# Kernel tuning notes

Hardware: AMD Instinct MI355X
Metric: run time of the kernel (lower is better)

The kernel has to match this reference:

```python
import jax, jax.numpy as jnp
import numpy as np

MAX_DISP = 48


def setup_inputs() -> dict:
    key = jax.random.key(0)
    k1, k2 = jax.random.split(key)
    n, c, h, w = 2, 32, 136, 240
    left = jax.random.normal(k1, (n, c, h, w), dtype=jnp.float32)
    right = jax.random.normal(k2, (n, c, h, w), dtype=jnp.float32)
    return {"left": left, "right": right}


def _cost_volume(left, right, max_disp):
    # volume[n, c, d, h, w] = left[n,c,h,w] * right[n,c,h,w-d] for w >= d, else 0
    w = left.shape[-1]
    slices = []
    for d in range(max_disp):
        # shift right feature map by d along W, zero-padding on the left;
        # the zero pad makes volume[..., :d] zero automatically, matching the
        # torch loop that only writes volume[:, :, d, :, d:].
        shifted = jnp.pad(right, ((0, 0), (0, 0), (0, 0), (d, 0)))[..., :w]
        slices.append(left * shifted)
    return jnp.stack(slices, axis=2)  # N x C x D x H x W


def reference(left, right):
    return _cost_volume(left, right, MAX_DISP)
```

## Files before the change

kernel.cpp:

```cpp
#include <hip/hip_runtime.h>


constexpr int W   = 240;
constexpr int H   = 136;
constexpr int D   = 48;
constexpr int W4  = W / 4;
constexpr int HW4 = H * W4;

typedef float v4f __attribute__((ext_vector_type(4)));

__global__ __launch_bounds__(256) void cost_volume_kernel(
    const float* __restrict__ left,
    const float* __restrict__ right,
    float* __restrict__ out)
{
    const int d  = blockIdx.x;
    const int nc = blockIdx.y;

    const float* __restrict__ L = left  + (size_t)nc * (H * W);
    const float* __restrict__ R = right + (size_t)nc * (H * W);
    v4f* __restrict__ O = reinterpret_cast<v4f*>(out) + ((size_t)nc * D + d) * (size_t)HW4;

    for (int i = threadIdx.x; i < HW4; i += 256) {
        const int h   = (unsigned)i / W4;
        const int w4  = i - h * W4;
        const int row = h * W;

        const v4f l = *reinterpret_cast<const v4f*>(L + row + 4 * w4);

        const int off = 4 * w4 - d;
        const float r0 = R[row + ((off + 0 >= 0) ? off + 0 : 0)];
        const float r1 = R[row + ((off + 1 >= 0) ? off + 1 : 0)];
        const float r2 = R[row + ((off + 2 >= 0) ? off + 2 : 0)];
        const float r3 = R[row + ((off + 3 >= 0) ? off + 3 : 0)];

        v4f v;
        v.x = (off + 0 >= 0) ? l.x * r0 : 0.f;
        v.y = (off + 1 >= 0) ? l.y * r1 : 0.f;
        v.z = (off + 2 >= 0) ? l.z * r2 : 0.f;
        v.w = (off + 3 >= 0) ? l.w * r3 : 0.f;
        O[i] = v;
    }
}

extern "C" void kernel_launch(void* const* d_in, const int* in_sizes, int n_in,
                              void* d_out, int out_size, void* d_ws, size_t ws_size,
                              hipStream_t stream) {
    const float* left  = (const float*)d_in[0];
    const float* right = (const float*)d_in[1];
    float* out = (float*)d_out;
    const int rows = in_sizes[0] / W;
    const int nc   = rows / H;
    dim3 grid(D, nc);
    cost_volume_kernel<<<grid, 256, 0, stream>>>(left, right, out);
}
```

Before: 510.5 us.

## Flatten output indexing into fixed-size chunks per block with interior fast path

Replaces the (disparity, n*c) grid with a 1D grid where each block covers a contiguous chunk of 48*256 output vec4s. Each element's nc, d, h and w4 come from integer divisions. For interior columns (w4>=12) the right-operand gather drops the clamp/select logic and reads four consecutive floats. This balances work across blocks and cuts per-element ALU on a store-bound kernel, at the cost of extra index divisions per element.

```diff
diff --git a/kernel.cpp b/kernel.cpp
--- a/kernel.cpp
+++ b/kernel.cpp
@@ -1,45 +1,65 @@
 #include <hip/hip_runtime.h>
 
 
-constexpr int W   = 240;
-constexpr int H   = 136;
-constexpr int D   = 48;
-constexpr int W4  = W / 4;
-constexpr int HW4 = H * W4;
+constexpr int W    = 240;
+constexpr int H    = 136;
+constexpr int D    = 48;
+constexpr int W4   = W / 4;
+constexpr int HW4  = H * W4;
+constexpr int DHW4 = D * HW4;
+constexpr int ITERS  = 48;
+constexpr int CHUNK4 = ITERS * 256;
 
 typedef float v4f __attribute__((ext_vector_type(4)));
+typedef float v2f __attribute__((ext_vector_type(2)));
 
 __global__ __launch_bounds__(256) void cost_volume_kernel(
     const float* __restrict__ left,
     const float* __restrict__ right,
-    float* __restrict__ out)
+    float* __restrict__ out,
+    int total4)
 {
-    const int d  = blockIdx.x;
-    const int nc = blockIdx.y;
+    const int base = blockIdx.x * CHUNK4 + threadIdx.x;
+    v4f* __restrict__ O = reinterpret_cast<v4f*>(out);
 
-    const float* __restrict__ L = left  + (size_t)nc * (H * W);
-    const float* __restrict__ R = right + (size_t)nc * (H * W);
-    v4f* __restrict__ O = reinterpret_cast<v4f*>(out) + ((size_t)nc * D + d) * (size_t)HW4;
+    #pragma unroll 2
+    for (int it = 0; it < ITERS; ++it) {
+        const int i = base + it * 256;
+        if (i >= total4) return;
 
-    for (int i = threadIdx.x; i < HW4; i += 256) {
-        const int h   = (unsigned)i / W4;
-        const int w4  = i - h * W4;
-        const int row = h * W;
+        const unsigned u   = (unsigned)i;
+        const unsigned nc  = u / (unsigned)DHW4;
+        const unsigned rem1 = u - nc * DHW4;
+        const unsigned d   = rem1 / (unsigned)HW4;
+        const unsigned rem2 = rem1 - d * HW4;
+        const unsigned h   = rem2 / (unsigned)W4;
+        const unsigned w4  = rem2 - h * W4;
 
-        const v4f l = *reinterpret_cast<const v4f*>(L + row + 4 * w4);
+        const unsigned row  = (nc * H + h) * W;
+        const unsigned loff = row + 4 * w4;
 
-        const int off = 4 * w4 - d;
-        const float r0 = R[row + ((off + 0 >= 0) ? off + 0 : 0)];
-        const float r1 = R[row + ((off + 1 >= 0) ? off + 1 : 0)];
-        const float r2 = R[row + ((off + 2 >= 0) ? off + 2 : 0)];
-        const float r3 = R[row + ((off + 3 >= 0) ? off + 3 : 0)];
+        const v4f l4 = *reinterpret_cast<const v4f*>(left + loff);
 
-        v4f v;
-        v.x = (off + 0 >= 0) ? l.x * r0 : 0.f;
-        v.y = (off + 1 >= 0) ? l.y * r1 : 0.f;
-        v.z = (off + 2 >= 0) ? l.z * r2 : 0.f;
-        v.w = (off + 3 >= 0) ? l.w * r3 : 0.f;
-        O[i] = v;
+        v4f r;
+        if (w4 >= 12) {
+            const float* __restrict__ Rp = right + (loff - d);
+            r.x = Rp[0];
+            r.y = Rp[1];
+            r.z = Rp[2];
+            r.w = Rp[3];
+        } else {
+            const int off = (int)(4 * w4) - (int)d;
+            const float* __restrict__ Rr = right + row;
+            const float e0 = Rr[(off + 0 >= 0) ? off + 0 : 0];
+            const float e1 = Rr[(off + 1 >= 0) ? off + 1 : 0];
+            const float e2 = Rr[(off + 2 >= 0) ? off + 2 : 0];
+            const float e3 = Rr[(off + 3 >= 0) ? off + 3 : 0];
+            r.x = (off + 0 >= 0) ? e0 : 0.f;
+            r.y = (off + 1 >= 0) ? e1 : 0.f;
+            r.z = (off + 2 >= 0) ? e2 : 0.f;
+            r.w = (off + 3 >= 0) ? e3 : 0.f;
+        }
+        O[i] = l4 * r;
     }
 }
 
@@ -49,8 +69,9 @@
     const float* left  = (const float*)d_in[0];
     const float* right = (const float*)d_in[1];
     float* out = (float*)d_out;
-    const int rows = in_sizes[0] / W;
-    const int nc   = rows / H;
-    dim3 grid(D, nc);
-    cost_volume_kernel<<<grid, 256, 0, stream>>>(left, right, out);
+    const int rows   = in_sizes[0] / W;
+    const int nc     = rows / H;
+    const int total4 = nc * DHW4;
+    const int nblocks = (total4 + CHUNK4 - 1) / CHUNK4;
+    cost_volume_kernel<<<nblocks, 256, 0, stream>>>(left, right, out, total4);
 }
```

Result: faster. 451.6 us (-11.5%).
